# Kernel tuning notes

Measured on AMD Instinct MI355X. Metric: run time of the kernel, lower is better.

## Reference

```python
import jax, jax.numpy as jnp
import numpy as np

NUM_MAPS = 512
NUM_BLOCKS = 2
ZG = 512
HID = min(96, NUM_MAPS)          # shared query / attention hidden dim
SEQ = 8                           # hardcoded inner sequence length
H1 = min(NUM_MAPS // 32, 3)       # num_heads1 = 3
H2 = NUM_MAPS // 32               # num_heads2 = 16
NPROC = NUM_BLOCKS * 4            # 4 FiLM param types per block


def _mha(q, k, v, nheads):
    """Multi-head attention. q:(Lq,D) k,v:(Lk,D) -> (Lq,D)."""
    Lq, D = q.shape
    Lk = k.shape[0]
    d = D // nheads
    qh = q.reshape(Lq, nheads, d).transpose(1, 0, 2)   # (h,Lq,d)
    kh = k.reshape(Lk, nheads, d).transpose(1, 0, 2)
    vh = v.reshape(Lk, nheads, d).transpose(1, 0, 2)
    A = jax.nn.softmax(jnp.einsum('hqd,hkd->hqk', qh, kh) / jnp.sqrt(jnp.asarray(D, q.dtype)))
    O = jnp.einsum('hqk,hkd->hqd', A, vh)
    return O.transpose(1, 0, 2).reshape(Lq, D)


def setup_inputs() -> dict:
    key = jax.random.key(0)
    ks = jax.random.split(key, 20)
    s = 0.05
    n = jax.random.normal
    return {
        'gate': jax.random.uniform(ks[0], (1, SEQ), dtype=jnp.float32),
        'x': n(ks[1], (1, ZG), dtype=jnp.float32),
        # shared_layer_alphaC : Linear(ZG, NUM_MAPS) + Sigmoid
        'Wa': n(ks[2], (ZG, NUM_MAPS)) * s, 'ba': jnp.zeros((NUM_MAPS,)),
        # shared_layer_Query : Linear(ZG, HID) + ReLU
        'Wqr': n(ks[3], (ZG, HID)) * s, 'bqr': jnp.zeros((HID,)),
        # stacked FiLM params: [block, {g1,b1,g2,b2}, num_maps, 8]
        'P': n(ks[4], (NUM_BLOCKS, 4, NUM_MAPS, SEQ)) * 0.2,
        'De': n(ks[5], (NUM_BLOCKS, 4, NUM_MAPS, SEQ)) * 0.01,
        'regs': n(ks[6], (NUM_BLOCKS, 4, NUM_MAPS)) * 0.001,
        # SMAB_small processor weights, stacked over the 8 processors
        'Wq1': n(ks[7], (NPROC, NUM_MAPS, HID)) * s,
        'Wk1': n(ks[8], (NPROC, NUM_MAPS, HID)) * s,
        'Wv1': n(ks[9], (NPROC, NUM_MAPS, HID)) * s,
        'fc1': n(ks[10], (NPROC, HID, HID)) * s,
        'Wq2': n(ks[11], (NPROC, HID, HID)) * s,
        'Wk2': n(ks[12], (NPROC, HID, HID)) * s,
        'Wv2': n(ks[13], (NPROC, HID, HID)) * s,
        'fc2': n(ks[14], (NPROC, HID, HID)) * s,
        'Wo': n(ks[15], (NPROC, HID, NUM_MAPS)) * s,
    }


def reference(gate, x, Wa, ba, Wqr, bqr, P, De, regs,
              Wq1, Wk1, Wv1, fc1, Wq2, Wk2, Wv2, fc2, Wo):
    alpha = jax.nn.sigmoid(x @ Wa + ba).reshape(-1)        # (NUM_MAPS,)
    q = jax.nn.relu(x @ Wqr + bqr)                          # (1, HID)

    # per-processor key/value set: transpose(1,0).view(1,8,num_maps)
    K_all = P.reshape(NPROC, NUM_MAPS, SEQ).transpose(0, 2, 1)  # (8procs, 8, NUM_MAPS)

    def smab(K, wq1, wk1, wv1, f1, wq2, wk2, wv2, f2, wo):
        # stage 1: self-attention over the 8-element set (num_heads1)
        Qk = K @ wq1                                        # (8, HID)
        H = Qk + _mha(Qk, K @ wk1, K @ wv1, H1)
        H = H + jax.nn.relu(H @ f1)
        # stage 2: task query attends to the set (num_heads2)
        Qq = q @ wq2                                        # (1, HID)
        O = Qq + _mha(Qq, H @ wk2, H @ wv2, H2)
        O = O + jax.nn.relu(O @ f2)
        return (O @ wo)[0]                                  # (NUM_MAPS,)

    trans = jax.vmap(smab)(K_all, Wq1, Wk1, Wv1, fc1, Wq2, Wk2, Wv2, fc2, Wo)
    trans = trans.reshape(NUM_BLOCKS, 4, NUM_MAPS)

    de = (De * gate[0]).sum(-1)                             # (NB,4,NUM_MAPS)
    mix = alpha * trans + (1.0 - alpha) * de
    offs = jnp.array([1.0, 0.0, 1.0, 0.0], dtype=mix.dtype).reshape(1, 4, 1)
    # gamma gets +1 offset, beta does not
    return mix * regs + offs
```

## Files before the change

kernel.cpp:

```cpp
#include <hip/hip_runtime.h>
#include <hip/hip_bf16.h>
#include <math.h>


#define WS_ALPHA 0
#define WS_Q     512
#define WS_QKV   608
#define WS_K2    19040
#define WS_V2    25184
#define WS_QQ    31328

__global__ __launch_bounds__(256) void kA_qkv_alpha_q(
    const float* __restrict__ x, const float* __restrict__ Wa,
    const float* __restrict__ ba, const float* __restrict__ Wqr,
    const float* __restrict__ bqr, const float* __restrict__ P,
    const float* __restrict__ Wq1, const float* __restrict__ Wk1,
    const float* __restrict__ Wv1, float* __restrict__ ws)
{
    __shared__ float sK[8 * 528];
    __shared__ float sp[2048];
    const int blk = blockIdx.x, tid = threadIdx.x;

    if (blk < 144) {
        const int proc = blk & 7, rem = blk >> 3;
        const int mat = rem / 6, six = rem % 6;
        const int hl = tid & 15, ks = tid >> 4;
        const int h = six * 16 + hl;
        const float* W = (mat == 0 ? Wq1 : (mat == 1 ? Wk1 : Wv1))
                         + proc * 49152 + (ks * 32) * 96 + h;
        float wreg[32];
        #pragma unroll
        for (int m2 = 0; m2 < 32; ++m2) wreg[m2] = W[m2 * 96];
        const float4* P4 = (const float4*)(P + proc * 4096);
        for (int i = tid; i < 1024; i += 256) {
            float4 v = P4[i];
            const int c = i >> 1, off = (i & 1) * 4;
            const int cp = c + (c >> 5);
            sK[(off + 0) * 528 + cp] = v.x;
            sK[(off + 1) * 528 + cp] = v.y;
            sK[(off + 2) * 528 + cp] = v.z;
            sK[(off + 3) * 528 + cp] = v.w;
        }
        __syncthreads();
        const float* Kb = sK + ks * 33;
        float acc[8] = {0.f,0.f,0.f,0.f,0.f,0.f,0.f,0.f};
        #pragma unroll
        for (int m2 = 0; m2 < 32; ++m2) {
            const float w = wreg[m2];
            const float* Kc = Kb + m2;
            #pragma unroll
            for (int s = 0; s < 8; ++s) acc[s] += Kc[s * 528] * w;
        }
        float* spb = sp + ks * 128 + hl * 8;
        #pragma unroll
        for (int s = 0; s < 8; ++s) spb[s] = acc[s];
        __syncthreads();
        if (tid < 128) {
            float a = 0.f;
            #pragma unroll
            for (int u = 0; u < 16; ++u) a += sp[u * 128 + tid];
            const int hl2 = tid >> 3, s = tid & 7;
            ws[WS_QKV + proc * 2304 + mat * 768 + s * 96 + six * 16 + hl2] = a;
        }
    } else if (blk < 176) {
        const int ml = tid & 15, ks = tid >> 4;
        const int m = (blk - 144) * 16 + ml;
        const float* W = Wa + (ks * 32) * 512 + m;
        float wreg[32];
        #pragma unroll
        for (int k = 0; k < 32; ++k) wreg[k] = W[k * 512];
        for (int k = tid; k < 512; k += 256) sK[k] = x[k];
        __syncthreads();
        const float* xq = sK + ks * 32;
        float acc = 0.f;
        #pragma unroll
        for (int k = 0; k < 32; ++k) acc += xq[k] * wreg[k];
        sp[tid] = acc;
        __syncthreads();
        if (tid < 16) {
            float a = ba[(blk - 144) * 16 + tid];
            #pragma unroll
            for (int u = 0; u < 16; ++u) a += sp[u * 16 + tid];
            ws[WS_ALPHA + (blk - 144) * 16 + tid] = 1.f / (1.f + __expf(-a));
        }
    } else {
        const int hl = tid & 15, ks = tid >> 4;
        const int h = (blk - 176) * 16 + hl;
        const float* W = Wqr + (ks * 32) * 96 + h;
        float wreg[32];
        #pragma unroll
        for (int k = 0; k < 32; ++k) wreg[k] = W[k * 96];
        for (int k = tid; k < 512; k += 256) sK[k] = x[k];
        __syncthreads();
        const float* xq = sK + ks * 32;
        float acc = 0.f;
        #pragma unroll
        for (int k = 0; k < 32; ++k) acc += xq[k] * wreg[k];
        sp[tid] = acc;
        __syncthreads();
        if (tid < 16) {
            float a = bqr[(blk - 176) * 16 + tid];
            #pragma unroll
            for (int u = 0; u < 16; ++u) a += sp[u * 16 + tid];
            ws[WS_Q + (blk - 176) * 16 + tid] = fmaxf(a, 0.f);
        }
    }
}

__global__ __launch_bounds__(256) void kB_attn1_fc1_kv2(
    const float* __restrict__ fc1w, const float* __restrict__ Wk2,
    const float* __restrict__ Wv2, const float* __restrict__ Wq2,
    float* __restrict__ ws)
{
    const int b = blockIdx.x, tid = threadIdx.x;
    const float rs = 0.10206207261596577f;

    if (b < 48) {
        const int proc = b & 7, slot = b >> 3;
        const int mat = slot / 3, t = slot % 3;
        __shared__ float sQk[768], sKk[768], sVv[768], sH[768], sH2[768], sS[192];
        __shared__ float sWf1[9216];
        __shared__ float sWkv[96 * 32];

        {
            const float4* F4 = (const float4*)fc1w + proc * 2304;
            float4* D4 = (float4*)sWf1;
            #pragma unroll
            for (int r = 0; r < 9; ++r) D4[tid + 256 * r] = F4[tid + 256 * r];
            const float4* KV4 = (const float4*)(mat ? Wv2 : Wk2);
            float4* E4 = (float4*)sWkv;
            #pragma unroll
            for (int r = 0; r < 3; ++r) {
                const int idx = tid + 256 * r;
                const int row = idx >> 3, q4 = idx & 7;
                E4[row * 8 + q4] = KV4[proc * 2304 + row * 24 + t * 8 + q4];
            }
        }
        const float* qkv = ws + WS_QKV + proc * 2304;
        for (int i = tid; i < 768; i += 256) {
            sQk[i] = qkv[i]; sKk[i] = qkv[768 + i]; sVv[i] = qkv[1536 + i];
        }
        __syncthreads();

        if (tid < 192) {
            const int h0 = tid / 64, r64 = tid % 64, si = r64 / 8, sk = r64 % 8;
            float acc = 0.f;
            #pragma unroll
            for (int d = 0; d < 32; ++d)
                acc += sQk[si * 96 + h0 * 32 + d] * sKk[sk * 96 + h0 * 32 + d];
            sS[tid] = acc * rs;
        }
        __syncthreads();
        if (tid < 24) {
            float* row = sS + tid * 8;
            float mx = row[0];
            #pragma unroll
            for (int k = 1; k < 8; ++k) mx = fmaxf(mx, row[k]);
            float e[8], sum = 0.f;
            #pragma unroll
            for (int k = 0; k < 8; ++k) { e[k] = __expf(row[k] - mx); sum += e[k]; }
            const float inv = 1.f / sum;
            #pragma unroll
            for (int k = 0; k < 8; ++k) row[k] = e[k] * inv;
        }
        __syncthreads();
        if (tid < 192) {
            const int h0 = tid / 64, r64 = tid % 64, si = r64 / 8, dq = r64 % 8;
            const float* e = sS + h0 * 64 + si * 8;
            float o0 = 0.f, o1 = 0.f, o2 = 0.f, o3 = 0.f;
            #pragma unroll
            for (int k = 0; k < 8; ++k) {
                const float ek = e[k];
                const float* v = sVv + k * 96 + h0 * 32 + dq * 4;
                o0 += ek*v[0]; o1 += ek*v[1]; o2 += ek*v[2]; o3 += ek*v[3];
            }
            const int base = si * 96 + h0 * 32 + dq * 4;
            sH[base+0] = sQk[base+0] + o0;  sH[base+1] = sQk[base+1] + o1;
            sH[base+2] = sQk[base+2] + o2;  sH[base+3] = sQk[base+3] + o3;
        }
        __syncthreads();
        #pragma unroll
        for (int r = 0; r < 3; ++r) {
            const int idx = tid + 256 * r, s = idx / 96, j = idx % 96;
            const float* Hs = sH + s * 96;
            float acc = 0.f;
            #pragma unroll
            for (int i = 0; i < 96; ++i) acc += Hs[i] * sWf1[i * 96 + j];
            sH2[idx] = sH[idx] + fmaxf(acc, 0.f);
        }
        __syncthreads();
        const int s = tid >> 5, jl = tid & 31, j = t * 32 + jl;
        const float* Hs = sH2 + s * 96;
        float acc = 0.f;
        #pragma unroll
        for (int i = 0; i < 96; ++i) acc += Hs[i] * sWkv[i * 32 + jl];
        ws[(mat ? WS_V2 : WS_K2) + proc * 768 + s * 96 + j] = acc;
    } else {
        const int b2 = b - 48, proc = b2 & 7, t = b2 >> 3;
        __shared__ float sq[96], sp[256];
        if (tid < 96) sq[tid] = ws[WS_Q + tid];
        __syncthreads();
        const int jl = tid & 31, ks = tid >> 5;
        const int j = 32 * t + jl;
        const float* W = Wq2 + proc * 9216 + j;
        float acc = 0.f;
        #pragma unroll
        for (int i = 0; i < 12; ++i)
            acc += sq[12 * ks + i] * W[(12 * ks + i) * 96];
        sp[tid] = acc;
        __syncthreads();
        if (ks == 0) {
            float a = 0.f;
            #pragma unroll
            for (int u = 0; u < 8; ++u) a += sp[jl + 32 * u];
            ws[WS_QQ + proc * 96 + j] = a;
        }
    }
}

__global__ __launch_bounds__(256) void kC_attn2_fc2_out(
    const float* __restrict__ gate, const float* __restrict__ De,
    const float* __restrict__ regs, const float* __restrict__ fc2w,
    const float* __restrict__ Wo, const float* __restrict__ ws,
    float* __restrict__ out)
{
    const int b = blockIdx.x, proc = b & 7, e = b >> 3, tid = threadIdx.x;
    __shared__ float sK2[768], sV2[768];
    __shared__ float sQq[96], sO[96], sOf[96], sE2[128], sg[8], sp[256];
    __shared__ float sWf2[9216];
    __shared__ float sWo[96 * 64];
    const float rs = 0.10206207261596577f;

    {
        const float4* F4 = (const float4*)fc2w + proc * 2304;
        float4* D4 = (float4*)sWf2;
        #pragma unroll
        for (int r = 0; r < 9; ++r) D4[tid + 256 * r] = F4[tid + 256 * r];
        const float4* W4 = (const float4*)Wo;
        float4* E4 = (float4*)sWo;
        #pragma unroll
        for (int r = 0; r < 6; ++r) {
            const int idx = tid + 256 * r;
            const int row = idx >> 4, q4 = idx & 15;
            E4[row * 16 + q4] = W4[proc * 12288 + row * 128 + e * 16 + q4];
        }
    }
    const int ml = tid & 63, ks = tid >> 6;
    const int m = 64 * e + ml;
    const float4* Dp4 = (const float4*)(De + proc * 4096 + m * 8);
    const float4 d0 = Dp4[0], d1 = Dp4[1];
    const float av = ws[WS_ALPHA + m];
    const float rg = regs[proc * 512 + m];
    for (int i = tid; i < 768; i += 256) {
        sK2[i] = ws[WS_K2 + proc * 768 + i];
        sV2[i] = ws[WS_V2 + proc * 768 + i];
    }
    if (tid < 96) sQq[tid] = ws[WS_QQ + proc * 96 + tid];
    else if (tid >= 96 && tid < 104) sg[tid - 96] = gate[tid - 96];
    __syncthreads();

    if (tid < 16) {
        const int h0 = tid;
        float lg[8], mx = -1e30f;
        #pragma unroll
        for (int k = 0; k < 8; ++k) {
            float acc = 0.f;
            #pragma unroll
            for (int d = 0; d < 6; ++d)
                acc += sQq[h0 * 6 + d] * sK2[k * 96 + h0 * 6 + d];
            lg[k] = acc * rs; mx = fmaxf(mx, lg[k]);
        }
        float ex[8], sum = 0.f;
        #pragma unroll
        for (int k = 0; k < 8; ++k) { ex[k] = __expf(lg[k] - mx); sum += ex[k]; }
        const float inv = 1.f / sum;
        #pragma unroll
        for (int k = 0; k < 8; ++k) sE2[h0 * 8 + k] = ex[k] * inv;
    }
    __syncthreads();
    if (tid < 96) {
        const int h0 = tid / 6;
        float o = 0.f;
        #pragma unroll
        for (int k = 0; k < 8; ++k) o += sE2[h0 * 8 + k] * sV2[k * 96 + tid];
        sO[tid] = sQq[tid] + o;
    }
    __syncthreads();
    if (tid < 192) {
        const int j = tid % 96, k2 = tid / 96;
        const float* Os = sO + k2 * 48;
        float acc = 0.f;
        #pragma unroll
        for (int i = 0; i < 48; ++i) acc += Os[i] * sWf2[(k2 * 48 + i) * 96 + j];
        sp[tid] = acc;
    }
    __syncthreads();
    if (tid < 96) sOf[tid] = sO[tid] + fmaxf(sp[tid] + sp[96 + tid], 0.f);
    __syncthreads();

    float acc = 0.f;
    #pragma unroll
    for (int i = 0; i < 24; ++i)
        acc += sOf[24 * ks + i] * sWo[(24 * ks + i) * 64 + ml];
    sp[tid] = acc;
    __syncthreads();
    if (ks == 0) {
        const float tr = sp[ml] + sp[ml + 64] + sp[ml + 128] + sp[ml + 192];
        const float de = d0.x * sg[0] + d0.y * sg[1] + d0.z * sg[2] + d0.w * sg[3]
                       + d1.x * sg[4] + d1.y * sg[5] + d1.z * sg[6] + d1.w * sg[7];
        const float mix = av * tr + (1.f - av) * de;
        const int pt = proc & 3;
        const float off = (pt == 0 || pt == 2) ? 1.f : 0.f;
        out[proc * 512 + m] = mix * rg + off;
    }
}

extern "C" void kernel_launch(void* const* d_in, const int* in_sizes, int n_in,
                              void* d_out, int out_size, void* d_ws, size_t ws_size,
                              hipStream_t stream)
{
    const float* gate = (const float*)d_in[0];
    const float* x    = (const float*)d_in[1];
    const float* Wa   = (const float*)d_in[2];
    const float* ba   = (const float*)d_in[3];
    const float* Wqr  = (const float*)d_in[4];
    const float* bqr  = (const float*)d_in[5];
    const float* P    = (const float*)d_in[6];
    const float* De   = (const float*)d_in[7];
    const float* regs = (const float*)d_in[8];
    const float* Wq1  = (const float*)d_in[9];
    const float* Wk1  = (const float*)d_in[10];
    const float* Wv1  = (const float*)d_in[11];
    const float* fc1  = (const float*)d_in[12];
    const float* Wq2  = (const float*)d_in[13];
    const float* Wk2  = (const float*)d_in[14];
    const float* Wv2  = (const float*)d_in[15];
    const float* fc2  = (const float*)d_in[16];
    const float* Wo   = (const float*)d_in[17];
    float* ws = (float*)d_ws;

    hipLaunchKernelGGL(kA_qkv_alpha_q, dim3(182), dim3(256), 0, stream,
                       x, Wa, ba, Wqr, bqr, P, Wq1, Wk1, Wv1, ws);
    hipLaunchKernelGGL(kB_attn1_fc1_kv2, dim3(72), dim3(256), 0, stream,
                       fc1, Wk2, Wv2, Wq2, ws);
    hipLaunchKernelGGL(kC_attn2_fc2_out, dim3(64), dim3(256), 0, stream,
                       gate, De, regs, fc2, Wo, ws, (float*)d_out);
}
```

Measured before the change: 108.3 us.

## Fuse three kernels into one cooperative kernel with grid syncs and weight prefetch

Merges the three sequential launches into a single cooperative kernel of 254 blocks separated by two grid-wide barriers. Blocks that are idle in early phases preload their later-phase weights (fc1, Wk2/Wv2, Wq2, fc2, Wo, De) into shared memory or registers before the barrier, so weight fetch overlaps the earlier stages. This removes two kernel launch gaps and hides weight-load latency, in exchange for the cost of grid syncs and a larger shared-memory footprint per block.

```diff
diff --git a/kernel.cpp b/kernel.cpp
--- a/kernel.cpp
+++ b/kernel.cpp
@@ -1,6 +1,8 @@
 #include <hip/hip_runtime.h>
-#include <hip/hip_bf16.h>
+#include <hip/hip_cooperative_groups.h>
 #include <math.h>
+
+namespace cg = cooperative_groups;
 
 
 #define WS_ALPHA 0
@@ -10,19 +12,29 @@
 #define WS_V2    25184
 #define WS_QQ    31328
 
-__global__ __launch_bounds__(256) void kA_qkv_alpha_q(
-    const float* __restrict__ x, const float* __restrict__ Wa,
-    const float* __restrict__ ba, const float* __restrict__ Wqr,
-    const float* __restrict__ bqr, const float* __restrict__ P,
+__global__ __launch_bounds__(256) void fused_film(
+    const float* __restrict__ gate, const float* __restrict__ x,
+    const float* __restrict__ Wa,  const float* __restrict__ ba,
+    const float* __restrict__ Wqr, const float* __restrict__ bqr,
+    const float* __restrict__ P,   const float* __restrict__ De,
+    const float* __restrict__ regs,
     const float* __restrict__ Wq1, const float* __restrict__ Wk1,
-    const float* __restrict__ Wv1, float* __restrict__ ws)
+    const float* __restrict__ Wv1, const float* __restrict__ fc1w,
+    const float* __restrict__ Wq2, const float* __restrict__ Wk2,
+    const float* __restrict__ Wv2, const float* __restrict__ fc2w,
+    const float* __restrict__ Wo,
+    float* __restrict__ ws, float* __restrict__ out)
 {
-    __shared__ float sK[8 * 528];
-    __shared__ float sp[2048];
-    const int blk = blockIdx.x, tid = threadIdx.x;
-
-    if (blk < 144) {
-        const int proc = blk & 7, rem = blk >> 3;
+    __shared__ float lds[16320];
+    const int bid = blockIdx.x, tid = threadIdx.x;
+    const float rs = 0.10206207261596577f;
+
+    float wq2r[12];
+
+    if (bid < 144) {
+        float* sK = lds;
+        float* sp = lds + 4224;
+        const int proc = bid & 7, rem = bid >> 3;
         const int mat = rem / 6, six = rem % 6;
         const int hl = tid & 15, ks = tid >> 4;
         const int h = six * 16 + hl;
@@ -62,67 +74,59 @@
             const int hl2 = tid >> 3, s = tid & 7;
             ws[WS_QKV + proc * 2304 + mat * 768 + s * 96 + six * 16 + hl2] = a;
         }
-    } else if (blk < 176) {
+    } else if (bid < 176) {
+        float* xb = lds;
+        float* sp = lds + 4224;
         const int ml = tid & 15, ks = tid >> 4;
-        const int m = (blk - 144) * 16 + ml;
+        const int m = (bid - 144) * 16 + ml;
         const float* W = Wa + (ks * 32) * 512 + m;
         float wreg[32];
         #pragma unroll
         for (int k = 0; k < 32; ++k) wreg[k] = W[k * 512];
-        for (int k = tid; k < 512; k += 256) sK[k] = x[k];
-        __syncthreads();
-        const float* xq = sK + ks * 32;
+        for (int k = tid; k < 512; k += 256) xb[k] = x[k];
+        __syncthreads();
+        const float* xq = xb + ks * 32;
         float acc = 0.f;
         #pragma unroll
         for (int k = 0; k < 32; ++k) acc += xq[k] * wreg[k];
         sp[tid] = acc;
         __syncthreads();
         if (tid < 16) {
-            float a = ba[(blk - 144) * 16 + tid];
+            float a = ba[(bid - 144) * 16 + tid];
             #pragma unroll
             for (int u = 0; u < 16; ++u) a += sp[u * 16 + tid];
-            ws[WS_ALPHA + (blk - 144) * 16 + tid] = 1.f / (1.f + __expf(-a));
-        }
-    } else {
+            ws[WS_ALPHA + (bid - 144) * 16 + tid] = 1.f / (1.f + __expf(-a));
+        }
+    } else if (bid < 182) {
+        float* xb = lds;
+        float* sp = lds + 4224;
         const int hl = tid & 15, ks = tid >> 4;
-        const int h = (blk - 176) * 16 + hl;
+        const int h = (bid - 176) * 16 + hl;
         const float* W = Wqr + (ks * 32) * 96 + h;
         float wreg[32];
         #pragma unroll
         for (int k = 0; k < 32; ++k) wreg[k] = W[k * 96];
-        for (int k = tid; k < 512; k += 256) sK[k] = x[k];
-        __syncthreads();
-        const float* xq = sK + ks * 32;
+        for (int k = tid; k < 512; k += 256) xb[k] = x[k];
+        __syncthreads();
+        const float* xq = xb + ks * 32;
         float acc = 0.f;
         #pragma unroll
         for (int k = 0; k < 32; ++k) acc += xq[k] * wreg[k];
         sp[tid] = acc;
         __syncthreads();
         if (tid < 16) {
-            float a = bqr[(blk - 176) * 16 + tid];
+            float a = bqr[(bid - 176) * 16 + tid];
             #pragma unroll
             for (int u = 0; u < 16; ++u) a += sp[u * 16 + tid];
-            ws[WS_Q + (blk - 176) * 16 + tid] = fmaxf(a, 0.f);
-        }
-    }
-}
-
-__global__ __launch_bounds__(256) void kB_attn1_fc1_kv2(
-    const float* __restrict__ fc1w, const float* __restrict__ Wk2,
-    const float* __restrict__ Wv2, const float* __restrict__ Wq2,
-    float* __restrict__ ws)
-{
-    const int b = blockIdx.x, tid = threadIdx.x;
-    const float rs = 0.10206207261596577f;
-
-    if (b < 48) {
-        const int proc = b & 7, slot = b >> 3;
-        const int mat = slot / 3, t = slot % 3;
-        __shared__ float sQk[768], sKk[768], sVv[768], sH[768], sH2[768], sS[192];
-        __shared__ float sWf1[9216];
-        __shared__ float sWkv[96 * 32];
-
-        {
+            ws[WS_Q + (bid - 176) * 16 + tid] = fmaxf(a, 0.f);
+        }
+    } else {
+        const int rb = bid - 182;
+        if (rb < 48) {
+            const int proc = rb & 7, slot = rb >> 3;
+            const int mat = slot / 3, t = slot % 3;
+            float* sWf1 = lds;
+            float* sWkv = lds + 9216;
             const float4* F4 = (const float4*)fc1w + proc * 2304;
             float4* D4 = (float4*)sWf1;
             #pragma unroll
@@ -135,183 +139,207 @@
                 const int row = idx >> 3, q4 = idx & 7;
                 E4[row * 8 + q4] = KV4[proc * 2304 + row * 24 + t * 8 + q4];
             }
-        }
-        const float* qkv = ws + WS_QKV + proc * 2304;
-        for (int i = tid; i < 768; i += 256) {
-            sQk[i] = qkv[i]; sKk[i] = qkv[768 + i]; sVv[i] = qkv[1536 + i];
-        }
-        __syncthreads();
-
-        if (tid < 192) {
-            const int h0 = tid / 64, r64 = tid % 64, si = r64 / 8, sk = r64 % 8;
+        } else {
+            const int rq = rb - 48, proc = rq & 7, t = rq >> 3;
+            const int jl = tid & 31, ks8 = tid >> 5;
+            const int j = 32 * t + jl;
+            const float* W = Wq2 + proc * 9216 + j;
+            #pragma unroll
+            for (int i = 0; i < 12; ++i) wq2r[i] = W[(12 * ks8 + i) * 96];
+        }
+    }
+
+    cg::this_grid().sync();
+
+    float wor[24];
+    float der[8] = {0,0,0,0,0,0,0,0};
+    float av = 0.f, rg = 0.f;
+    if (bid >= 182) {
+        const int rb = bid - 182;
+        if (rb < 48) {
+            const int proc = rb & 7, slot = rb >> 3;
+            const int mat = slot / 3, t = slot % 3;
+            float* sWf1 = lds;
+            float* sWkv = lds + 9216;
+            float* sQk = lds + 12288;
+            float* sKk = lds + 13056;
+            float* sVv = lds + 13824;
+            float* sH  = lds + 14592;
+            float* sH2 = lds + 15360;
+            float* sS  = lds + 16128;
+            const float* qkv = ws + WS_QKV + proc * 2304;
+            for (int i = tid; i < 768; i += 256) {
+                sQk[i] = qkv[i]; sKk[i] = qkv[768 + i]; sVv[i] = qkv[1536 + i];
+            }
+            __syncthreads();
+            if (tid < 192) {
+                const int h0 = tid / 64, r64 = tid % 64, si = r64 / 8, sk = r64 % 8;
+                float acc = 0.f;
+                #pragma unroll
+                for (int d = 0; d < 32; ++d)
+                    acc += sQk[si * 96 + h0 * 32 + d] * sKk[sk * 96 + h0 * 32 + d];
+                sS[tid] = acc * rs;
+            }
+            __syncthreads();
+            if (tid < 24) {
+                float* row = sS + tid * 8;
+                float mx = row[0];
+                #pragma unroll
+                for (int k = 1; k < 8; ++k) mx = fmaxf(mx, row[k]);
+                float e[8], sum = 0.f;
+                #pragma unroll
+                for (int k = 0; k < 8; ++k) { e[k] = __expf(row[k] - mx); sum += e[k]; }
+                const float inv = 1.f / sum;
+                #pragma unroll
+                for (int k = 0; k < 8; ++k) row[k] = e[k] * inv;
+            }
+            __syncthreads();
+            if (tid < 192) {
+                const int h0 = tid / 64, r64 = tid % 64, si = r64 / 8, dq = r64 % 8;
+                const float* e = sS + h0 * 64 + si * 8;
+                float o0 = 0.f, o1 = 0.f, o2 = 0.f, o3 = 0.f;
+                #pragma unroll
+                for (int k = 0; k < 8; ++k) {
+                    const float ek = e[k];
+                    const float* v = sVv + k * 96 + h0 * 32 + dq * 4;
+                    o0 += ek*v[0]; o1 += ek*v[1]; o2 += ek*v[2]; o3 += ek*v[3];
+                }
+                const int base = si * 96 + h0 * 32 + dq * 4;
+                sH[base+0] = sQk[base+0] + o0;  sH[base+1] = sQk[base+1] + o1;
+                sH[base+2] = sQk[base+2] + o2;  sH[base+3] = sQk[base+3] + o3;
+            }
+            __syncthreads();
+            #pragma unroll
+            for (int r = 0; r < 3; ++r) {
+                const int idx = tid + 256 * r, s = idx / 96, j = idx % 96;
+                const float* Hs = sH + s * 96;
+                float acc = 0.f;
+                #pragma unroll
+                for (int i = 0; i < 96; ++i) acc += Hs[i] * sWf1[i * 96 + j];
+                sH2[idx] = sH[idx] + fmaxf(acc, 0.f);
+            }
+            __syncthreads();
+            const int s = tid >> 5, jl = tid & 31, j = t * 32 + jl;
+            const float* Hs = sH2 + s * 96;
             float acc = 0.f;
             #pragma unroll
-            for (int d = 0; d < 32; ++d)
-                acc += sQk[si * 96 + h0 * 32 + d] * sKk[sk * 96 + h0 * 32 + d];
-            sS[tid] = acc * rs;
-        }
-        __syncthreads();
-        if (tid < 24) {
-            float* row = sS + tid * 8;
-            float mx = row[0];
-            #pragma unroll
-            for (int k = 1; k < 8; ++k) mx = fmaxf(mx, row[k]);
-            float e[8], sum = 0.f;
-            #pragma unroll
-            for (int k = 0; k < 8; ++k) { e[k] = __expf(row[k] - mx); sum += e[k]; }
-            const float inv = 1.f / sum;
-            #pragma unroll
-            for (int k = 0; k < 8; ++k) row[k] = e[k] * inv;
-        }
-        __syncthreads();
-        if (tid < 192) {
-            const int h0 = tid / 64, r64 = tid % 64, si = r64 / 8, dq = r64 % 8;
-            const float* e = sS + h0 * 64 + si * 8;
-            float o0 = 0.f, o1 = 0.f, o2 = 0.f, o3 = 0.f;
-            #pragma unroll
-            for (int k = 0; k < 8; ++k) {
-                const float ek = e[k];
-                const float* v = sVv + k * 96 + h0 * 32 + dq * 4;
-                o0 += ek*v[0]; o1 += ek*v[1]; o2 += ek*v[2]; o3 += ek*v[3];
-            }
-            const int base = si * 96 + h0 * 32 + dq * 4;
-            sH[base+0] = sQk[base+0] + o0;  sH[base+1] = sQk[base+1] + o1;
-            sH[base+2] = sQk[base+2] + o2;  sH[base+3] = sQk[base+3] + o3;
-        }
-        __syncthreads();
-        #pragma unroll
-        for (int r = 0; r < 3; ++r) {
-            const int idx = tid + 256 * r, s = idx / 96, j = idx % 96;
-            const float* Hs = sH + s * 96;
+            for (int i = 0; i < 96; ++i) acc += Hs[i] * sWkv[i * 32 + jl];
+            ws[(mat ? WS_V2 : WS_K2) + proc * 768 + s * 96 + j] = acc;
+        } else {
+            const int rq = rb - 48, proc = rq & 7, t = rq >> 3;
+            float* sq  = lds;
+            float* spq = lds + 96;
+            if (tid < 96) sq[tid] = ws[WS_Q + tid];
+            __syncthreads();
+            const int jl = tid & 31, ks8 = tid >> 5;
+            const int j = 32 * t + jl;
             float acc = 0.f;
             #pragma unroll
-            for (int i = 0; i < 96; ++i) acc += Hs[i] * sWf1[i * 96 + j];
-            sH2[idx] = sH[idx] + fmaxf(acc, 0.f);
-        }
-        __syncthreads();
-        const int s = tid >> 5, jl = tid & 31, j = t * 32 + jl;
-        const float* Hs = sH2 + s * 96;
-        float acc = 0.f;
-        #pragma unroll
-        for (int i = 0; i < 96; ++i) acc += Hs[i] * sWkv[i * 32 + jl];
-        ws[(mat ? WS_V2 : WS_K2) + proc * 768 + s * 96 + j] = acc;
-    } else {
-        const int b2 = b - 48, proc = b2 & 7, t = b2 >> 3;
-        __shared__ float sq[96], sp[256];
-        if (tid < 96) sq[tid] = ws[WS_Q + tid];
-        __syncthreads();
-        const int jl = tid & 31, ks = tid >> 5;
-        const int j = 32 * t + jl;
-        const float* W = Wq2 + proc * 9216 + j;
-        float acc = 0.f;
-        #pragma unroll
-        for (int i = 0; i < 12; ++i)
-            acc += sq[12 * ks + i] * W[(12 * ks + i) * 96];
-        sp[tid] = acc;
-        __syncthreads();
-        if (ks == 0) {
-            float a = 0.f;
-            #pragma unroll
-            for (int u = 0; u < 8; ++u) a += sp[jl + 32 * u];
-            ws[WS_QQ + proc * 96 + j] = a;
-        }
-    }
-}
-
-__global__ __launch_bounds__(256) void kC_attn2_fc2_out(
-    const float* __restrict__ gate, const float* __restrict__ De,
-    const float* __restrict__ regs, const float* __restrict__ fc2w,
-    const float* __restrict__ Wo, const float* __restrict__ ws,
-    float* __restrict__ out)
-{
-    const int b = blockIdx.x, proc = b & 7, e = b >> 3, tid = threadIdx.x;
-    __shared__ float sK2[768], sV2[768];
-    __shared__ float sQq[96], sO[96], sOf[96], sE2[128], sg[8], sp[256];
-    __shared__ float sWf2[9216];
-    __shared__ float sWo[96 * 64];
-    const float rs = 0.10206207261596577f;
-
-    {
+            for (int i = 0; i < 12; ++i) acc += sq[12 * ks8 + i] * wq2r[i];
+            spq[tid] = acc;
+            __syncthreads();
+            if (ks8 == 0) {
+                float a = 0.f;
+                #pragma unroll
+                for (int u = 0; u < 8; ++u) a += spq[jl + 32 * u];
+                ws[WS_QQ + proc * 96 + j] = a;
+            }
+        }
+    } else if (bid < 64) {
+        const int proc = bid & 7, e = bid >> 3;
+        float* sWf2 = lds;
+        float* sg   = lds + 11168;
         const float4* F4 = (const float4*)fc2w + proc * 2304;
         float4* D4 = (float4*)sWf2;
         #pragma unroll
         for (int r = 0; r < 9; ++r) D4[tid + 256 * r] = F4[tid + 256 * r];
-        const float4* W4 = (const float4*)Wo;
-        float4* E4 = (float4*)sWo;
-        #pragma unroll
-        for (int r = 0; r < 6; ++r) {
-            const int idx = tid + 256 * r;
-            const int row = idx >> 4, q4 = idx & 15;
-            E4[row * 16 + q4] = W4[proc * 12288 + row * 128 + e * 16 + q4];
-        }
+        const int ml = tid & 63, ksv = tid >> 6;
+        const int m = 64 * e + ml;
+        const float* Wop = Wo + proc * 49152 + m;
+        #pragma unroll
+        for (int i = 0; i < 24; ++i) wor[i] = Wop[(24 * ksv + i) * 512];
+        const float4* Dp4 = (const float4*)(De + proc * 4096 + m * 8);
+        const float4 t0 = Dp4[0], t1 = Dp4[1];
+        der[0]=t0.x; der[1]=t0.y; der[2]=t0.z; der[3]=t0.w;
+        der[4]=t1.x; der[5]=t1.y; der[6]=t1.z; der[7]=t1.w;
+        av = ws[WS_ALPHA + m];
+        rg = regs[proc * 512 + m];
+        if (tid < 8) sg[tid] = gate[tid];
     }
-    const int ml = tid & 63, ks = tid >> 6;
-    const int m = 64 * e + ml;
-    const float4* Dp4 = (const float4*)(De + proc * 4096 + m * 8);
-    const float4 d0 = Dp4[0], d1 = Dp4[1];
-    const float av = ws[WS_ALPHA + m];
-    const float rg = regs[proc * 512 + m];
-    for (int i = tid; i < 768; i += 256) {
-        sK2[i] = ws[WS_K2 + proc * 768 + i];
-        sV2[i] = ws[WS_V2 + proc * 768 + i];
-    }
-    if (tid < 96) sQq[tid] = ws[WS_QQ + proc * 96 + tid];
-    else if (tid >= 96 && tid < 104) sg[tid - 96] = gate[tid - 96];
-    __syncthreads();
-
-    if (tid < 16) {
-        const int h0 = tid;
-        float lg[8], mx = -1e30f;
-        #pragma unroll
-        for (int k = 0; k < 8; ++k) {
+
+    cg::this_grid().sync();
+
+    if (bid < 64) {
+        const int proc = bid & 7, e = bid >> 3;
+        float* sWf2 = lds;
+        float* sK2 = lds + 9216;
+        float* sV2 = lds + 9984;
+        float* sQq = lds + 10752;
+        float* sO  = lds + 10848;
+        float* sOf = lds + 10944;
+        float* sE2 = lds + 11040;
+        float* sg  = lds + 11168;
+        float* spc = lds + 11176;
+        const int ml = tid & 63, ksv = tid >> 6;
+        const int m = 64 * e + ml;
+        for (int i = tid; i < 768; i += 256) {
+            sK2[i] = ws[WS_K2 + proc * 768 + i];
+            sV2[i] = ws[WS_V2 + proc * 768 + i];
+        }
+        if (tid < 96) sQq[tid] = ws[WS_QQ + proc * 96 + tid];
+        __syncthreads();
+        if (tid < 16) {
+            const int h0 = tid;
+            float lg[8], mx = -1e30f;
+            #pragma unroll
+            for (int k = 0; k < 8; ++k) {
+                float acc = 0.f;
+                #pragma unroll
+                for (int d = 0; d < 6; ++d)
+                    acc += sQq[h0 * 6 + d] * sK2[k * 96 + h0 * 6 + d];
+                lg[k] = acc * rs; mx = fmaxf(mx, lg[k]);
+            }
+            float ex[8], sum = 0.f;
+            #pragma unroll
+            for (int k = 0; k < 8; ++k) { ex[k] = __expf(lg[k] - mx); sum += ex[k]; }
+            const float inv = 1.f / sum;
+            #pragma unroll
+            for (int k = 0; k < 8; ++k) sE2[h0 * 8 + k] = ex[k] * inv;
+        }
+        __syncthreads();
+        if (tid < 96) {
+            const int h0 = tid / 6;
+            float o = 0.f;
+            #pragma unroll
+            for (int k = 0; k < 8; ++k) o += sE2[h0 * 8 + k] * sV2[k * 96 + tid];
+            sO[tid] = sQq[tid] + o;
+        }
+        __syncthreads();
+        if (tid < 192) {
+            const int j = tid % 96, k2 = tid / 96;
+            const float* Os = sO + k2 * 48;
             float acc = 0.f;
             #pragma unroll
-            for (int d = 0; d < 6; ++d)
-                acc += sQq[h0 * 6 + d] * sK2[k * 96 + h0 * 6 + d];
-            lg[k] = acc * rs; mx = fmaxf(mx, lg[k]);
-        }
-        float ex[8], sum = 0.f;
-        #pragma unroll
-        for (int k = 0; k < 8; ++k) { ex[k] = __expf(lg[k] - mx); sum += ex[k]; }
-        const float inv = 1.f / sum;
-        #pragma unroll
-        for (int k = 0; k < 8; ++k) sE2[h0 * 8 + k] = ex[k] * inv;
-    }
-    __syncthreads();
-    if (tid < 96) {
-        const int h0 = tid / 6;
-        float o = 0.f;
-        #pragma unroll
-        for (int k = 0; k < 8; ++k) o += sE2[h0 * 8 + k] * sV2[k * 96 + tid];
-        sO[tid] = sQq[tid] + o;
-    }
-    __syncthreads();
-    if (tid < 192) {
-        const int j = tid % 96, k2 = tid / 96;
-        const float* Os = sO + k2 * 48;
+            for (int i = 0; i < 48; ++i) acc += Os[i] * sWf2[(k2 * 48 + i) * 96 + j];
+            spc[tid] = acc;
+        }
+        __syncthreads();
+        if (tid < 96) sOf[tid] = sO[tid] + fmaxf(spc[tid] + spc[96 + tid], 0.f);
+        __syncthreads();
         float acc = 0.f;
         #pragma unroll
-        for (int i = 0; i < 48; ++i) acc += Os[i] * sWf2[(k2 * 48 + i) * 96 + j];
-        sp[tid] = acc;
-    }
-    __syncthreads();
-    if (tid < 96) sOf[tid] = sO[tid] + fmaxf(sp[tid] + sp[96 + tid], 0.f);
-    __syncthreads();
-
-    float acc = 0.f;
-    #pragma unroll
-    for (int i = 0; i < 24; ++i)
-        acc += sOf[24 * ks + i] * sWo[(24 * ks + i) * 64 + ml];
-    sp[tid] = acc;
-    __syncthreads();
-    if (ks == 0) {
-        const float tr = sp[ml] + sp[ml + 64] + sp[ml + 128] + sp[ml + 192];
-        const float de = d0.x * sg[0] + d0.y * sg[1] + d0.z * sg[2] + d0.w * sg[3]
-                       + d1.x * sg[4] + d1.y * sg[5] + d1.z * sg[6] + d1.w * sg[7];
-        const float mix = av * tr + (1.f - av) * de;
-        const int pt = proc & 3;
-        const float off = (pt == 0 || pt == 2) ? 1.f : 0.f;
-        out[proc * 512 + m] = mix * rg + off;
+        for (int i = 0; i < 24; ++i) acc += sOf[24 * ksv + i] * wor[i];
+        spc[tid] = acc;
+        __syncthreads();
+        if (ksv == 0) {
+            const float tr = spc[ml] + spc[ml + 64] + spc[ml + 128] + spc[ml + 192];
+            const float de = der[0]*sg[0] + der[1]*sg[1] + der[2]*sg[2] + der[3]*sg[3]
+                           + der[4]*sg[4] + der[5]*sg[5] + der[6]*sg[6] + der[7]*sg[7];
+            const float mix = av * tr + (1.f - av) * de;
+            const int pt = proc & 3;
+            const float off = (pt == 0 || pt == 2) ? 1.f : 0.f;
+            out[proc * 512 + m] = mix * rg + off;
+        }
     }
 }
 
@@ -337,12 +365,15 @@
     const float* Wv2  = (const float*)d_in[15];
     const float* fc2  = (const float*)d_in[16];
     const float* Wo   = (const float*)d_in[17];
-    float* ws = (float*)d_ws;
-
-    hipLaunchKernelGGL(kA_qkv_alpha_q, dim3(182), dim3(256), 0, stream,
-                       x, Wa, ba, Wqr, bqr, P, Wq1, Wk1, Wv1, ws);
-    hipLaunchKernelGGL(kB_attn1_fc1_kv2, dim3(72), dim3(256), 0, stream,
-                       fc1, Wk2, Wv2, Wq2, ws);
-    hipLaunchKernelGGL(kC_attn2_fc2_out, dim3(64), dim3(256), 0, stream,
-                       gate, De, regs, fc2, Wo, ws, (float*)d_out);
+    float* ws   = (float*)d_ws;
+    float* outp = (float*)d_out;
+
+    void* args[] = {
+        (void*)&gate, (void*)&x, (void*)&Wa, (void*)&ba, (void*)&Wqr, (void*)&bqr,
+        (void*)&P, (void*)&De, (void*)&regs, (void*)&Wq1, (void*)&Wk1, (void*)&Wv1,
+        (void*)&fc1, (void*)&Wq2, (void*)&Wk2, (void*)&Wv2, (void*)&fc2, (void*)&Wo,
+        (void*)&ws, (void*)&outp
+    };
+    hipLaunchCooperativeKernel((void*)fused_film, dim3(254), dim3(256),
+                               args, 0, stream);
 }
```

Result: slower. 189.9 us (+75.4%).
